# Performance work log

Hardware: AMD Instinct MI355X
Metric: run time of the kernel (lower is better)

## Reference

```python
import math
import jax, jax.numpy as jnp
import numpy as np

B, N, D, H, P = 16, 500, 32, 128, 100
E = N * D
N_HEADS, QKV = 8, 16
TANH_CLIP = 10.0

def setup_inputs() -> dict:
    key = jax.random.key(0)
    ks = jax.random.split(key, 16)
    emb = jax.random.normal(ks[0], (B, E, H), jnp.float32)
    dists = jax.random.uniform(ks[1], (B, N, N, 2), jnp.float32)
    pref = jax.random.uniform(ks[2], (2,), jnp.float32)
    # regular edge list: node i owns edges [i*D, (i+1)*D); dst random in [0,N)
    src = jnp.broadcast_to(jnp.arange(E, dtype=jnp.int32) // D, (B, E))
    dst = jax.random.randint(ks[3], (B, E), 0, N, dtype=jnp.int32)
    indices = jnp.stack([src, dst], axis=-1)
    w = lambda k: jax.random.normal(k, (H, H), jnp.float32) * 0.05
    return {
        'embeddings': emb,
        'dists': dists,
        'pref': pref,
        'indices': indices,
        'Wq_first': w(ks[4]), 'Wq_last': w(ks[5]), 'Wq_visited': w(ks[6]),
        'Wq_graph': w(ks[7]), 'Wq': w(ks[8]), 'Wk': w(ks[9]),
        'q_first': jax.random.normal(ks[10], (B, P, H), jnp.float32),
        'visited_embedding': jnp.zeros((B, P, H), jnp.float32),
        'last_edge_embedding': jax.random.normal(ks[11], (B, P, H), jnp.float32),
        'last_node_index': jax.random.randint(ks[12], (B, P), 0, N, dtype=jnp.int32),
        'group_ninf_mask': jnp.zeros((B, P, N), jnp.float32),
    }

def reference(embeddings, dists, pref, indices, Wq_first, Wq_last, Wq_visited,
              Wq_graph, Wq, Wk, q_first, visited_embedding, last_edge_embedding,
              last_node_index, group_ninf_mask):
    Bsz, Etot, Hd = embeddings.shape
    Nn = dists.shape[1]
    Deg = Etot // Nn
    # combined objective (training_method == 'Linear')
    dists_c = pref[0] * dists[..., 0] + pref[1] * dists[..., 1]  # [B,N,N]
    # outgoing edge ids of each current node (regular degree -> contiguous block)
    out_idx = last_node_index[:, :, None].astype(jnp.int32) * Deg + jnp.arange(Deg, dtype=jnp.int32)  # [B,P,D]
    bidx = jnp.arange(Bsz)[:, None, None]
    outgoing_embeddings = embeddings[bidx, out_idx]          # [B,P,D,H]
    node_keys = indices[bidx, out_idx, 1]                    # [B,P,D] dst nodes
    # queries (q_first already set -> add_more_query path)
    q_graph = jnp.mean(embeddings, axis=1, keepdims=True) @ Wq_graph.T   # [B,1,H]
    q_last = last_edge_embedding @ Wq_last.T                 # [B,P,H]
    visited = visited_embedding + last_edge_embedding / Nn
    q_visited = visited @ Wq_visited.T
    final_q = q_last + q_first + q_graph + q_visited         # [B,P,H]
    # multi-head pointer attention over the D outgoing edges
    k = (outgoing_embeddings @ Wk.T).reshape(Bsz, -1, Deg, N_HEADS, QKV)   # [B,P,D,h,q]
    qh = (final_q @ Wq.T).reshape(Bsz, -1, N_HEADS, QKV)                    # [B,P,h,q]
    score = jnp.einsum('bpdhq,bphq->bhpd', k, qh) / math.sqrt(Hd)           # [B,h,P,D]
    distances = dists_c[jnp.arange(Bsz)[:, None], last_node_index]          # [B,P,N]
    d_sorted = jnp.take_along_axis(distances, node_keys, axis=2)            # [B,P,D]
    score = score - (d_sorted / math.sqrt(2.0))[:, None]
    score_clipped = TANH_CLIP * jnp.tanh(score.mean(axis=1))                # [B,P,D] (multi_pointer_level==1)
    mask = jnp.take_along_axis(group_ninf_mask, node_keys, axis=2)
    mask = jnp.where(jnp.isneginf(mask), jnp.float32(-1e8), mask)
    probs = jax.nn.softmax(score_clipped + mask, axis=-1)
    return probs, node_keys, outgoing_embeddings
```

## Files before the change

### kernel.cpp

```cpp
#include <hip/hip_runtime.h>
#include <hip/hip_bf16.h>
#include <math.h>

#define Bsz 16
#define Nn  500
#define Deg 32
#define Hd  128
#define Pg  100
#define Etot 16000
#define CHUNKS 64
#define ROWS_PER_CHUNK 250
#define PREP_BLKS 256

__global__ __launch_bounds__(256) void fused_all(const float* __restrict__ emb,
                                                 const float* __restrict__ wq,
                                                 const float* __restrict__ wk,
                                                 const float* __restrict__ wql,
                                                 const float* __restrict__ wqv,
                                                 const float* __restrict__ wqg,
                                                 float* __restrict__ partial,
                                                 float* __restrict__ mt,
                                                 float* __restrict__ at,
                                                 float* __restrict__ bt,
                                                 float* __restrict__ gt) {
    int blk = blockIdx.x;
    int tid = threadIdx.x;
    __shared__ float4 red[256];
    __shared__ float wv_s[2][Hd];

    if (blk >= PREP_BLKS) {
        int mb = blk - PREP_BLKS;
        int b = mb >> 6, chunk = mb & 63;
        int rgrp = tid >> 5, c4 = tid & 31;
        const float4* base = (const float4*)(emb + (size_t)b * Etot * Hd);
        int e0 = chunk * ROWS_PER_CHUNK;
        float4 acc = make_float4(0.f, 0.f, 0.f, 0.f);
        for (int e = e0 + rgrp; e < e0 + ROWS_PER_CHUNK; e += 8) {
            float4 v = base[(size_t)e * 32 + c4];
            acc.x += v.x; acc.y += v.y; acc.z += v.z; acc.w += v.w;
        }
        red[tid] = acc;
        __syncthreads();
        for (int s = 128; s >= 32; s >>= 1) {
            if (tid < s) {
                float4 a = red[tid], o = red[tid + s];
                a.x += o.x; a.y += o.y; a.z += o.z; a.w += o.w;
                red[tid] = a;
            }
            __syncthreads();
        }
        if (tid < 32)
            ((float4*)partial)[((size_t)b * CHUNKS + chunk) * 32 + tid] = red[tid];
        return;
    }

    int h = tid >> 7;
    int r = tid & 127;
    if (blk < 64) {
        int s = (blk << 1) | h;
        float acc = 0.f;
#pragma unroll 8
        for (int t = 0; t < Hd; ++t)
            acc += wq[t * Hd + s] * wk[t * Hd + r];
        mt[s * Hd + r] = acc;
        return;
    }
    int f = (blk - 64) >> 6;
    int u = (((blk - 64) & 63) << 1) | h;
    int t = r;
    float acc1 = 0.f;
    if (f == 0) {
#pragma unroll 8
        for (int s = 0; s < Hd; ++s)
            acc1 += (wql[s * Hd + u] + wqv[s * Hd + u] * (1.f / (float)Nn)) * wq[t * Hd + s];
    } else if (f == 1) {
#pragma unroll 8
        for (int s = 0; s < Hd; ++s)
            acc1 += wqv[s * Hd + u] * wq[t * Hd + s];
    } else {
#pragma unroll 8
        for (int s = 0; s < Hd; ++s)
            acc1 += wqg[s * Hd + u] * wq[t * Hd + s];
    }
    wv_s[h][t] = acc1;
    __syncthreads();
    float acc = 0.f;
#pragma unroll 8
    for (int tt = 0; tt < Hd; ++tt)
        acc += wv_s[h][tt] * wk[tt * Hd + r];
    float* dst = (f == 0) ? at : (f == 1) ? bt : gt;
    dst[u * Hd + r] = acc;
}

__global__ __launch_bounds__(256) void decode_z(const float* __restrict__ partial,
                                                const float* __restrict__ gt,
                                                const float* __restrict__ at,
                                                const float* __restrict__ bt,
                                                const float* __restrict__ mt,
                                                const float* __restrict__ qf,
                                                const float* __restrict__ vis,
                                                const float* __restrict__ le,
                                                const float* __restrict__ emb,
                                                const float* __restrict__ dists,
                                                const float* __restrict__ pref,
                                                const int* __restrict__ indices,
                                                const int* __restrict__ lni_arr,
                                                const float* __restrict__ gmask,
                                                float* __restrict__ out_probs,
                                                float* __restrict__ out_nk,
                                                float* __restrict__ out_og) {
    int blk = blockIdx.x;
    int b = blk / 50, p0 = (blk % 50) * 2;
    int bp0 = b * Pg + p0;
    int tid = threadIdx.x;

    __shared__ int lni_s[2];
    __shared__ float ps[2][Hd];
    __shared__ float mean_s[Hd];
    __shared__ __align__(16) float ins[Hd][3][2];
    __shared__ float zpart[2][2][Hd];
    __shared__ __align__(16) float z_s[2][Hd];
    __shared__ float score_s[2][Deg];

    if (tid < 2) lni_s[tid] = lni_arr[bp0 + tid];
    __syncthreads();

    int bp_i = tid >> 5, d = tid & 31;
    int nk = 0; float2 dd = make_float2(0.f, 0.f); float mval = 0.f;
    if (tid < 64) {
        int lnv = lni_s[bp_i];
        nk = indices[(((size_t)b * Etot) + (size_t)lnv * Deg + d) * 2 + 1];
        out_nk[(size_t)(bp0 + bp_i) * Deg + d] = (float)nk;
        dd = *(const float2*)(dists + (((size_t)b * Nn + (size_t)lnv) * Nn + nk) * 2);
        mval = gmask[(size_t)(bp0 + bp_i) * Nn + nk];
    }
    float p0v = pref[0], p1v = pref[1];

    {
        int c = tid & 127, h = tid >> 7;
        float s = 0.f;
        const float* pb = partial + (size_t)b * CHUNKS * Hd;
        for (int k = h * 32; k < h * 32 + 32; ++k)
            s += pb[k * Hd + c];
        ps[h][c] = s;
    }
    if (tid < 192) {
        size_t base4 = (size_t)bp0 * 32;
        const float4* le4 = (const float4*)le + base4;
        const float4* vi4 = (const float4*)vis + base4;
        const float4* qf4 = (const float4*)qf + base4;
        int m = tid / 64, idx = tid & 63;
        int bp = idx >> 5, cc4 = idx & 31;
        float4 v = (m == 0) ? le4[idx] : (m == 1) ? vi4[idx] : qf4[idx];
        int u0 = cc4 * 4;
        ins[u0 + 0][m][bp] = v.x;
        ins[u0 + 1][m][bp] = v.y;
        ins[u0 + 2][m][bp] = v.z;
        ins[u0 + 3][m][bp] = v.w;
    }
    __syncthreads();
    if (tid < Hd)
        mean_s[tid] = (ps[0][tid] + ps[1][tid]) * (1.f / (float)Etot);
    __syncthreads();

    {
        int r = tid & 127, h = tid >> 7;
        float acc0 = 0.f, acc1 = 0.f, accg = 0.f;
        const float* atp = at + r;
        const float* btp = bt + r;
        const float* mtp = mt + r;
        const float* gtp = gt + r;
#pragma unroll 4
        for (int u = h * 64; u < h * 64 + 64; ++u) {
            float wa = atp[u * Hd];
            float wb = btp[u * Hd];
            float wm = mtp[u * Hd];
            float wg = gtp[u * Hd];
            accg += wg * mean_s[u];
            float lv0 = ins[u][0][0], lv1 = ins[u][0][1];
            float vv0 = ins[u][1][0], vv1 = ins[u][1][1];
            float qv0 = ins[u][2][0], qv1 = ins[u][2][1];
            acc0 += wa * lv0 + wb * vv0 + wm * qv0;
            acc1 += wa * lv1 + wb * vv1 + wm * qv1;
        }
        zpart[h][0][r] = acc0 + accg;
        zpart[h][1][r] = acc1 + accg;
    }
    __syncthreads();
    {
        int bp = tid >> 7, r = tid & 127;
        z_s[bp][r] = zpart[0][bp][r] + zpart[1][bp][r];
    }
    __syncthreads();

    {
        int rg = tid >> 5, c4 = tid & 31;
        for (int bp = 0; bp < 2; ++bp) {
            const float4* ebase = (const float4*)emb + ((size_t)b * Etot + (size_t)lni_s[bp] * Deg) * 32;
            float4* ob = (float4*)out_og + ((size_t)(bp0 + bp)) * (Deg * 32);
            float4 z4 = ((const float4*)z_s[bp])[c4];
#pragma unroll
            for (int r0 = 0; r0 < 4; ++r0) {
                int r = rg + r0 * 8;
                float4 v = ebase[r * 32 + c4];
                ob[r * 32 + c4] = v;
                float part = v.x * z4.x + v.y * z4.y + v.z * z4.z + v.w * z4.w;
                for (int m = 16; m >= 1; m >>= 1)
                    part += __shfl_xor(part, m, 64);
                if (c4 == 0) score_s[bp][r] = part;
            }
        }
    }
    __syncthreads();

    if (tid < 64) {
        float s = score_s[bp_i][d] * 0.011048543456039805f;
        float ds = p0v * dd.x + p1v * dd.y;
        s -= ds * 0.7071067811865476f;
        float sc = 10.0f * tanhf(s);
        float m = mval;
        if (isinf(m) && m < 0.f) m = -1.0e8f;
        float v = sc + m;
        float mx = v;
        for (int mm = 16; mm >= 1; mm >>= 1)
            mx = fmaxf(mx, __shfl_xor(mx, mm, 64));
        float e = expf(v - mx);
        float sum = e;
        for (int mm = 16; mm >= 1; mm >>= 1)
            sum += __shfl_xor(sum, mm, 64);
        out_probs[(size_t)(bp0 + bp_i) * Deg + d] = e / sum;
    }
}

extern "C" void kernel_launch(void* const* d_in, const int* in_sizes, int n_in,
                              void* d_out, int out_size, void* d_ws, size_t ws_size,
                              hipStream_t stream) {
    const float* emb       = (const float*)d_in[0];
    const float* dists     = (const float*)d_in[1];
    const float* pref      = (const float*)d_in[2];
    const int*   indices   = (const int*)d_in[3];
    const float* Wq_last    = (const float*)d_in[5];
    const float* Wq_visited = (const float*)d_in[6];
    const float* Wq_graph   = (const float*)d_in[7];
    const float* Wq         = (const float*)d_in[8];
    const float* Wk         = (const float*)d_in[9];
    const float* q_first    = (const float*)d_in[10];
    const float* visited    = (const float*)d_in[11];
    const float* last_edge  = (const float*)d_in[12];
    const int*   lni        = (const int*)d_in[13];
    const float* gmask      = (const float*)d_in[14];

    float* w = (float*)d_ws;
    float* ws_partial = w;
    float* ws_mt      = ws_partial + (size_t)Bsz * CHUNKS * Hd;
    float* ws_at      = ws_mt + Hd * Hd;
    float* ws_bt      = ws_at + Hd * Hd;
    float* ws_gt      = ws_bt + Hd * Hd;

    float* out       = (float*)d_out;
    float* out_probs = out;
    float* out_nk    = out + (size_t)Bsz * Pg * Deg;
    float* out_og    = out + 2 * (size_t)Bsz * Pg * Deg;

    fused_all<<<PREP_BLKS + Bsz * CHUNKS, 256, 0, stream>>>(emb, Wq, Wk, Wq_last, Wq_visited,
                                                            Wq_graph, ws_partial, ws_mt,
                                                            ws_at, ws_bt, ws_gt);
    decode_z<<<800, 256, 0, stream>>>(ws_partial, ws_gt, ws_at, ws_bt, ws_mt,
                                      q_first, visited, last_edge, emb, dists, pref,
                                      indices, lni, gmask, out_probs, out_nk, out_og);
}
```

Before: 47.09 us.

## Pack precomputed weight products as bf16 pairs and merge prep blocks

The four precomputed 128x128 fused weight matrices (at, bt, mt, gt) are now stored as two arrays of packed bf16 pairs, which halves the weight bytes each decode block reads in its z projection loop. The prep work is regrouped so each block computes two matrices at once, sharing loads of Wq and Wk, and the prep block count drops from 256 to 128. The cost is reduced precision in the fused weights, rounded to bf16, which may perturb scores and probabilities slightly.

Result: faster. 45.52 us, median of 2 (-3.4%).

```diff
diff --git a/kernel.cpp b/kernel.cpp
--- a/kernel.cpp
+++ b/kernel.cpp
@@ -10,7 +10,13 @@
 #define Etot 16000
 #define CHUNKS 64
 #define ROWS_PER_CHUNK 250
-#define PREP_BLKS 256
+#define PREP_BLKS 128
+
+__device__ __forceinline__ unsigned pack_bf2(float a, float b) {
+    unsigned ua = (__float_as_uint(a) + 0x8000u) >> 16;
+    unsigned ub = (__float_as_uint(b) + 0x8000u) & 0xffff0000u;
+    return ua | ub;
+}
 
 __global__ __launch_bounds__(256) void fused_all(const float* __restrict__ emb,
                                                  const float* __restrict__ wq,
@@ -19,14 +25,12 @@
                                                  const float* __restrict__ wqv,
                                                  const float* __restrict__ wqg,
                                                  float* __restrict__ partial,
-                                                 float* __restrict__ mt,
-                                                 float* __restrict__ at,
-                                                 float* __restrict__ bt,
-                                                 float* __restrict__ gt) {
+                                                 unsigned* __restrict__ p1,
+                                                 unsigned* __restrict__ p2) {
     int blk = blockIdx.x;
     int tid = threadIdx.x;
     __shared__ float4 red[256];
-    __shared__ float wv_s[2][Hd];
+    __shared__ float wv_s[4][Hd];
 
     if (blk >= PREP_BLKS) {
         int mb = blk - PREP_BLKS;
@@ -57,46 +61,50 @@
     int h = tid >> 7;
     int r = tid & 127;
     if (blk < 64) {
-        int s = (blk << 1) | h;
-        float acc = 0.f;
-#pragma unroll 8
-        for (int t = 0; t < Hd; ++t)
-            acc += wq[t * Hd + s] * wk[t * Hd + r];
-        mt[s * Hd + r] = acc;
+        int u = (blk << 1) | h;
+        float accA = 0.f, accB = 0.f;
+#pragma unroll 8
+        for (int s = 0; s < Hd; ++s) {
+            float q = wq[r * Hd + s];
+            float wv = wqv[s * Hd + u];
+            accA += (wql[s * Hd + u] + wv * (1.f / (float)Nn)) * q;
+            accB += wv * q;
+        }
+        wv_s[h][r] = accA;
+        wv_s[2 + h][r] = accB;
+        __syncthreads();
+        float a2 = 0.f, b2 = 0.f;
+#pragma unroll 8
+        for (int tt = 0; tt < Hd; ++tt) {
+            float wkv = wk[tt * Hd + r];
+            a2 += wv_s[h][tt] * wkv;
+            b2 += wv_s[2 + h][tt] * wkv;
+        }
+        p1[u * Hd + r] = pack_bf2(a2, b2);
         return;
     }
-    int f = (blk - 64) >> 6;
-    int u = (((blk - 64) & 63) << 1) | h;
-    int t = r;
-    float acc1 = 0.f;
-    if (f == 0) {
+    {
+        int u = ((blk - 64) << 1) | h;
+        float accG = 0.f;
 #pragma unroll 8
         for (int s = 0; s < Hd; ++s)
-            acc1 += (wql[s * Hd + u] + wqv[s * Hd + u] * (1.f / (float)Nn)) * wq[t * Hd + s];
-    } else if (f == 1) {
-#pragma unroll 8
-        for (int s = 0; s < Hd; ++s)
-            acc1 += wqv[s * Hd + u] * wq[t * Hd + s];
-    } else {
-#pragma unroll 8
-        for (int s = 0; s < Hd; ++s)
-            acc1 += wqg[s * Hd + u] * wq[t * Hd + s];
-    }
-    wv_s[h][t] = acc1;
-    __syncthreads();
-    float acc = 0.f;
-#pragma unroll 8
-    for (int tt = 0; tt < Hd; ++tt)
-        acc += wv_s[h][tt] * wk[tt * Hd + r];
-    float* dst = (f == 0) ? at : (f == 1) ? bt : gt;
-    dst[u * Hd + r] = acc;
+            accG += wqg[s * Hd + u] * wq[r * Hd + s];
+        wv_s[h][r] = accG;
+        __syncthreads();
+        float m2 = 0.f, g2 = 0.f;
+#pragma unroll 8
+        for (int tt = 0; tt < Hd; ++tt) {
+            float wkv = wk[tt * Hd + r];
+            m2 += wq[tt * Hd + u] * wkv;
+            g2 += wv_s[h][tt] * wkv;
+        }
+        p2[u * Hd + r] = pack_bf2(m2, g2);
+    }
 }
 
 __global__ __launch_bounds__(256) void decode_z(const float* __restrict__ partial,
-                                                const float* __restrict__ gt,
-                                                const float* __restrict__ at,
-                                                const float* __restrict__ bt,
-                                                const float* __restrict__ mt,
+                                                const unsigned* __restrict__ p1,
+                                                const unsigned* __restrict__ p2,
                                                 const float* __restrict__ qf,
                                                 const float* __restrict__ vis,
                                                 const float* __restrict__ le,
@@ -166,16 +174,16 @@
     {
         int r = tid & 127, h = tid >> 7;
         float acc0 = 0.f, acc1 = 0.f, accg = 0.f;
-        const float* atp = at + r;
-        const float* btp = bt + r;
-        const float* mtp = mt + r;
-        const float* gtp = gt + r;
+        const unsigned* p1c = p1 + r;
+        const unsigned* p2c = p2 + r;
 #pragma unroll 4
         for (int u = h * 64; u < h * 64 + 64; ++u) {
-            float wa = atp[u * Hd];
-            float wb = btp[u * Hd];
-            float wm = mtp[u * Hd];
-            float wg = gtp[u * Hd];
+            unsigned w1 = p1c[u * Hd];
+            unsigned w2 = p2c[u * Hd];
+            float wa = __uint_as_float(w1 << 16);
+            float wb = __uint_as_float(w1 & 0xffff0000u);
+            float wm = __uint_as_float(w2 << 16);
+            float wg = __uint_as_float(w2 & 0xffff0000u);
             accg += wg * mean_s[u];
             float lv0 = ins[u][0][0], lv1 = ins[u][0][1];
             float vv0 = ins[u][1][0], vv1 = ins[u][1][1];
@@ -252,10 +260,8 @@
 
     float* w = (float*)d_ws;
     float* ws_partial = w;
-    float* ws_mt      = ws_partial + (size_t)Bsz * CHUNKS * Hd;
-    float* ws_at      = ws_mt + Hd * Hd;
-    float* ws_bt      = ws_at + Hd * Hd;
-    float* ws_gt      = ws_bt + Hd * Hd;
+    unsigned* ws_p1   = (unsigned*)(w + (size_t)Bsz * CHUNKS * Hd);
+    unsigned* ws_p2   = ws_p1 + Hd * Hd;
 
     float* out       = (float*)d_out;
     float* out_probs = out;
@@ -263,9 +269,8 @@
     float* out_og    = out + 2 * (size_t)Bsz * Pg * Deg;
 
     fused_all<<<PREP_BLKS + Bsz * CHUNKS, 256, 0, stream>>>(emb, Wq, Wk, Wq_last, Wq_visited,
-                                                            Wq_graph, ws_partial, ws_mt,
-                                                            ws_at, ws_bt, ws_gt);
-    decode_z<<<800, 256, 0, stream>>>(ws_partial, ws_gt, ws_at, ws_bt, ws_mt,
+                                                            Wq_graph, ws_partial, ws_p1, ws_p2);
+    decode_z<<<800, 256, 0, stream>>>(ws_partial, ws_p1, ws_p2,
                                       q_first, visited, last_edge, emb, dists, pref,
                                       indices, lni, gmask, out_probs, out_nk, out_og);
 }
```
